# Kernel optimization log

Hardware: AMD Instinct MI355X
Metric: run time of the kernel (lower is better)

The kernel has to match this reference:

```python
import jax, jax.numpy as jnp
import numpy as np

BN_EPS = 1e-5
OUT_H, OUT_W = 32, 32  # crop_size / output_stride = 512/16


def setup_inputs() -> dict:
    key = jax.random.key(0)
    k1, k2, k3, k4 = jax.random.split(key, 4)
    x = jax.random.normal(k1, (16, 2048, 32, 32), dtype=jnp.float32)
    # conv1x1 weight, bias-free: [dim_out, dim_in]
    W = jax.random.normal(k2, (256, 2048), dtype=jnp.float32) * (1.0 / np.sqrt(2048.0))
    gamma = jax.random.normal(k3, (256,), dtype=jnp.float32) * 0.1 + 1.0
    beta = jax.random.normal(k4, (256,), dtype=jnp.float32) * 0.1
    return {"x": x, "W": W, "gamma": gamma, "beta": beta}


def reference(x, W, gamma, beta):
    # 1x1 conv, no bias: channel contraction
    y = jnp.einsum("nchw,oc->nohw", x, W)  # [N, dim_out, H, W]
    # BatchNorm2d in training mode: batch statistics over (N, H, W), biased var
    mean = jnp.mean(y, axis=(0, 2, 3), keepdims=True)
    var = jnp.mean(jnp.square(y - mean), axis=(0, 2, 3), keepdims=True)
    g = gamma.reshape(1, -1, 1, 1)
    b = beta.reshape(1, -1, 1, 1)
    y = g * (y - mean) * jax.lax.rsqrt(var + BN_EPS) + b
    # global average pool to 1x1
    pooled = jnp.mean(y, axis=(2, 3), keepdims=True)  # [N, dim_out, 1, 1]
    # adaptive avg pool from 1x1 to (OUT_H, OUT_W) is a pure broadcast
    out = jnp.broadcast_to(pooled, pooled.shape[:2] + (OUT_H, OUT_W))
    return out
```

## Files before the change

### kernel.cpp

```cpp
#include <hip/hip_runtime.h>
#include <hip/hip_bf16.h>
#include <stdint.h>

#define NB   16
#define CIN  2048
#define OUTC 256
#define HW   1024
#define BJ   64
#define BK   32
#define NJT  (HW / BJ)
#define KSTEPS (CIN / BK)

typedef __attribute__((ext_vector_type(8))) short bf16x8;
typedef __attribute__((ext_vector_type(4))) float f32x4;
typedef __attribute__((ext_vector_type(4))) unsigned int u32x4;

__device__ __forceinline__ unsigned int f2bf(float f) {
    union { float f; unsigned int u; } a; a.f = f;
    return (a.u + 0x7FFFu + ((a.u >> 16) & 1u)) >> 16;
}

__device__ __forceinline__ void block_sync_lds() {
    asm volatile("s_waitcnt lgkmcnt(0)" ::: "memory");
    __builtin_amdgcn_s_barrier();
    asm volatile("" ::: "memory");
}

__global__ void wconv_kernel(const float* __restrict__ W, unsigned short* __restrict__ W16) {
    int i = (blockIdx.x * blockDim.x + threadIdx.x) * 4;
    float4 v = *reinterpret_cast<const float4*>(W + i);
    ushort4 o;
    o.x = (unsigned short)f2bf(v.x);
    o.y = (unsigned short)f2bf(v.y);
    o.z = (unsigned short)f2bf(v.z);
    o.w = (unsigned short)f2bf(v.w);
    *reinterpret_cast<ushort4*>(W16 + i) = o;
}

__global__ __launch_bounds__(512, 2) void gemm_stats_kernel(
    const float* __restrict__ x,
    const unsigned short* __restrict__ W16,
    float* __restrict__ s1_part,
    float* __restrict__ s2_part)
{
    __shared__ __align__(16) unsigned short A0[8192], A1[8192];
    __shared__ __align__(16) unsigned short B0[2048], B1[2048];

    const int tid  = threadIdx.x;
    const int lane = tid & 63;
    const int wave = tid >> 6;
    const int blk  = blockIdx.x;
    const int n    = blk >> 4;
    const int jt   = blk & 15;
    const int j0   = jt * BJ;

    const float* xn = x + (size_t)n * CIN * HW;

    const int arow  = tid >> 1;
    const int ahalf = tid & 1;
    const unsigned short* Agp = W16 + arow * CIN + ahalf * 16;
    const int offA0 = (arow >> 4) * 512 + (arow & 15) * 32 + ((2 * ahalf + 0) ^ (arow & 3)) * 8;
    const int offA1 = (arow >> 4) * 512 + (arow & 15) * 32 + ((2 * ahalf + 1) ^ (arow & 3)) * 8;

    const int bj = tid & 63;
    const int kh = tid >> 6;
    const float* Bgp = xn + (size_t)(kh * 4) * HW + j0 + bj;
    const int offB = (bj >> 4) * 512 + (bj & 15) * 32 + (((kh >> 1)) ^ (bj & 3)) * 8 + (kh & 1) * 4;

    const int rA = lane & 15;
    const int gX = (lane >> 4) ^ (rA & 3);
    const int roffA0 = (2 * wave) * 512 + rA * 32 + gX * 8;
    const int roffA1 = (2 * wave + 1) * 512 + rA * 32 + gX * 8;
    const int roffB  = rA * 32 + gX * 8;

#define LDA(ks, r0, r1) { r0 = *(const u32x4*)(Agp + (ks) * BK); \
                          r1 = *(const u32x4*)(Agp + (ks) * BK + 8); }
#define LDB(ks, f0, f1, f2, f3) { const float* p = Bgp + (size_t)(ks) * BK * HW; \
                                  f0 = p[0]; f1 = p[HW]; f2 = p[2 * HW]; f3 = p[3 * HW]; }
#define WRITE(Ab, Bb, r0, r1, f0, f1, f2, f3) { \
    *(u32x4*)&Ab[offA0] = r0; *(u32x4*)&Ab[offA1] = r1; \
    uint2 pk; pk.x = f2bf(f0) | (f2bf(f1) << 16); pk.y = f2bf(f2) | (f2bf(f3) << 16); \
    *(uint2*)&Bb[offB] = pk; }
#define COMPUTE(Ab, Bb) { \
    bf16x8 af0 = *(const bf16x8*)&Ab[roffA0]; \
    bf16x8 af1 = *(const bf16x8*)&Ab[roffA1]; \
    _Pragma("unroll") \
    for (int ni = 0; ni < 4; ++ni) { \
        bf16x8 bf = *(const bf16x8*)&Bb[ni * 512 + roffB]; \
        acc[0][ni] = __builtin_amdgcn_mfma_f32_16x16x32_bf16(af0, bf, acc[0][ni], 0, 0, 0); \
        acc[1][ni] = __builtin_amdgcn_mfma_f32_16x16x32_bf16(af1, bf, acc[1][ni], 0, 0, 0); \
    } }

    f32x4 acc[2][4] = {};
    u32x4 a00, a01, a10, a11;
    float b00, b01, b02, b03, b10, b11, b12, b13;

    LDA(0, a00, a01); LDB(0, b00, b01, b02, b03);
    LDA(1, a10, a11); LDB(1, b10, b11, b12, b13);
    WRITE(A0, B0, a00, a01, b00, b01, b02, b03);
    LDA(2, a00, a01); LDB(2, b00, b01, b02, b03);
    block_sync_lds();

    #pragma unroll 1
    for (int ks = 0; ks < KSTEPS; ks += 2) {
        COMPUTE(A0, B0);
        {
            WRITE(A1, B1, a10, a11, b10, b11, b12, b13);
            int kp = (ks + 3 < KSTEPS) ? ks + 3 : KSTEPS - 1;
            LDA(kp, a10, a11); LDB(kp, b10, b11, b12, b13);
            block_sync_lds();
        }
        COMPUTE(A1, B1);
        if (ks + 1 < KSTEPS - 1) {
            WRITE(A0, B0, a00, a01, b00, b01, b02, b03);
            int kp = (ks + 4 < KSTEPS) ? ks + 4 : KSTEPS - 1;
            LDA(kp, a00, a01); LDB(kp, b00, b01, b02, b03);
            block_sync_lds();
        }
    }

    float rs[2][4], rq[2][4];
    #pragma unroll
    for (int mi = 0; mi < 2; ++mi) {
        #pragma unroll
        for (int r = 0; r < 4; ++r) {
            float s = 0.f, q = 0.f;
            #pragma unroll
            for (int ni = 0; ni < 4; ++ni) {
                float v = acc[mi][ni][r];
                s += v; q += v * v;
            }
            rs[mi][r] = s; rq[mi][r] = q;
        }
    }
    #pragma unroll
    for (int m = 1; m < 16; m <<= 1) {
        #pragma unroll
        for (int mi = 0; mi < 2; ++mi) {
            #pragma unroll
            for (int r = 0; r < 4; ++r) {
                rs[mi][r] += __shfl_xor(rs[mi][r], m, 64);
                rq[mi][r] += __shfl_xor(rq[mi][r], m, 64);
            }
        }
    }
    if (rA == 0) {
        const int gK = lane >> 4;
        #pragma unroll
        for (int mi = 0; mi < 2; ++mi) {
            #pragma unroll
            for (int r = 0; r < 4; ++r) {
                int o = wave * 32 + mi * 16 + gK * 4 + r;
                s1_part[(jt * NB + n) * OUTC + o] = rs[mi][r];
                s2_part[blk * OUTC + o]           = rq[mi][r];
            }
        }
    }
#undef LDA
#undef LDB
#undef WRITE
#undef COMPUTE
}

__global__ __launch_bounds__(256) void finalize_bcast_kernel(
    const float* __restrict__ s1_part,
    const float* __restrict__ s2_part,
    const float* __restrict__ gamma,
    const float* __restrict__ beta,
    float* __restrict__ out)
{
    const int tid   = threadIdx.x;
    const int slice = tid & 15;
    const int o_l   = tid >> 4;
    const int n0    = blockIdx.x >> 4;
    const int o     = (blockIdx.x & 15) * 16 + o_l;

    float S1 = 0.f, S2 = 0.f;
    #pragma unroll
    for (int q = 0; q < 16; ++q) {
        int p = slice * 16 + q;
        S1 += s1_part[p * OUTC + o];
        S2 += s2_part[p * OUTC + o];
    }
    float s1n = s1_part[(slice * NB + n0) * OUTC + o];
    #pragma unroll
    for (int m = 1; m < 16; m <<= 1) {
        S1  += __shfl_xor(S1, m, 64);
        S2  += __shfl_xor(S2, m, 64);
        s1n += __shfl_xor(s1n, m, 64);
    }
    float mean = S1 * (1.f / 16384.f);
    float var  = S2 * (1.f / 16384.f) - mean * mean;
    float inv  = rsqrtf(var + 1e-5f);
    float v = gamma[o] * (s1n * (1.f / 1024.f) - mean) * inv + beta[o];

    float4 vv = make_float4(v, v, v, v);
    float4* dst = reinterpret_cast<float4*>(out + ((size_t)(n0 * OUTC + o)) * HW);
    #pragma unroll
    for (int it = 0; it < 16; ++it)
        dst[it * 16 + slice] = vv;
}

extern "C" void kernel_launch(void* const* d_in, const int* in_sizes, int n_in,
                              void* d_out, int out_size, void* d_ws, size_t ws_size,
                              hipStream_t stream) {
    const float* x     = (const float*)d_in[0];
    const float* W     = (const float*)d_in[1];
    const float* gamma = (const float*)d_in[2];
    const float* beta  = (const float*)d_in[3];
    float* out = (float*)d_out;

    char* ws = (char*)d_ws;
    unsigned short* W16 = (unsigned short*)ws;
    float* s1_part = (float*)(ws + (1 << 20));
    float* s2_part = (float*)(ws + (1 << 20) + (256 << 10));

    hipLaunchKernelGGL(wconv_kernel, dim3(512), dim3(256), 0, stream, W, W16);
    hipLaunchKernelGGL(gemm_stats_kernel, dim3(256), dim3(512), 0, stream,
                       x, W16, s1_part, s2_part);
    hipLaunchKernelGGL(finalize_bcast_kernel, dim3(NB * (OUTC / 16)), dim3(256), 0, stream,
                       s1_part, s2_part, gamma, beta, out);
}
```

Before: 56.02 us.

## Pre-swizzle weights into MFMA fragment layout and load A directly to registers

The weight prep kernel now writes bf16 weights in MFMA fragment order, so the GEMM kernel loads A operands straight from global/L2 into registers and no longer stages them through LDS. The K step doubles to 64, halving the number of barriers, and only the x tile is staged in LDS. This cuts LDS traffic and sync overhead but raises register use for the A fragments and the prefetched B values, and each block now fetches A directly from L2.

```diff
diff --git a/kernel.cpp b/kernel.cpp
--- a/kernel.cpp
+++ b/kernel.cpp
@@ -7,7 +7,7 @@
 #define OUTC 256
 #define HW   1024
 #define BJ   64
-#define BK   32
+#define BK   64
 #define NJT  (HW / BJ)
 #define KSTEPS (CIN / BK)
 
@@ -26,25 +26,29 @@
     asm volatile("" ::: "memory");
 }
 
-__global__ void wconv_kernel(const float* __restrict__ W, unsigned short* __restrict__ W16) {
-    int i = (blockIdx.x * blockDim.x + threadIdx.x) * 4;
-    float4 v = *reinterpret_cast<const float4*>(W + i);
-    ushort4 o;
-    o.x = (unsigned short)f2bf(v.x);
-    o.y = (unsigned short)f2bf(v.y);
-    o.z = (unsigned short)f2bf(v.z);
-    o.w = (unsigned short)f2bf(v.w);
-    *reinterpret_cast<ushort4*>(W16 + i) = o;
+__global__ void wprep_kernel(const float* __restrict__ W, unsigned short* __restrict__ Afrag) {
+    int g  = blockIdx.x * blockDim.x + threadIdx.x;
+    int o  = g >> 8;
+    int kc = g & 255;
+    const float4* p = reinterpret_cast<const float4*>(W + o * CIN + kc * 8);
+    float4 v0 = p[0], v1 = p[1];
+    u32x4 pk;
+    pk.x = f2bf(v0.x) | (f2bf(v0.y) << 16);
+    pk.y = f2bf(v0.z) | (f2bf(v0.w) << 16);
+    pk.z = f2bf(v1.x) | (f2bf(v1.y) << 16);
+    pk.w = f2bf(v1.z) | (f2bf(v1.w) << 16);
+    int ks32 = kc >> 2, g8 = kc & 3;
+    int lane = g8 * 16 + (o & 15), ot = o >> 4;
+    *reinterpret_cast<u32x4*>(Afrag + (((size_t)ks32 * 16 + ot) * 64 + lane) * 8) = pk;
 }
 
 __global__ __launch_bounds__(512, 2) void gemm_stats_kernel(
     const float* __restrict__ x,
-    const unsigned short* __restrict__ W16,
+    const unsigned short* __restrict__ Afrag,
     float* __restrict__ s1_part,
     float* __restrict__ s2_part)
 {
-    __shared__ __align__(16) unsigned short A0[8192], A1[8192];
-    __shared__ __align__(16) unsigned short B0[2048], B1[2048];
+    __shared__ __align__(16) unsigned short B0[4096], B1[4096];
 
     const int tid  = threadIdx.x;
     const int lane = tid & 63;
@@ -56,65 +60,66 @@
 
     const float* xn = x + (size_t)n * CIN * HW;
 
-    const int arow  = tid >> 1;
-    const int ahalf = tid & 1;
-    const unsigned short* Agp = W16 + arow * CIN + ahalf * 16;
-    const int offA0 = (arow >> 4) * 512 + (arow & 15) * 32 + ((2 * ahalf + 0) ^ (arow & 3)) * 8;
-    const int offA1 = (arow >> 4) * 512 + (arow & 15) * 32 + ((2 * ahalf + 1) ^ (arow & 3)) * 8;
-
     const int bj = tid & 63;
     const int kh = tid >> 6;
-    const float* Bgp = xn + (size_t)(kh * 4) * HW + j0 + bj;
-    const int offB = (bj >> 4) * 512 + (bj & 15) * 32 + (((kh >> 1)) ^ (bj & 3)) * 8 + (kh & 1) * 4;
+    const float* Bgp = xn + (size_t)(kh * 8) * HW + j0 + bj;
+    const int offB = (kh >> 2) * 2048 + (bj >> 4) * 512 + (bj & 15) * 32
+                   + ((kh & 3) ^ (bj & 3)) * 8;
 
     const int rA = lane & 15;
     const int gX = (lane >> 4) ^ (rA & 3);
-    const int roffA0 = (2 * wave) * 512 + rA * 32 + gX * 8;
-    const int roffA1 = (2 * wave + 1) * 512 + rA * 32 + gX * 8;
-    const int roffB  = rA * 32 + gX * 8;
-
-#define LDA(ks, r0, r1) { r0 = *(const u32x4*)(Agp + (ks) * BK); \
-                          r1 = *(const u32x4*)(Agp + (ks) * BK + 8); }
-#define LDB(ks, f0, f1, f2, f3) { const float* p = Bgp + (size_t)(ks) * BK * HW; \
-                                  f0 = p[0]; f1 = p[HW]; f2 = p[2 * HW]; f3 = p[3 * HW]; }
-#define WRITE(Ab, Bb, r0, r1, f0, f1, f2, f3) { \
-    *(u32x4*)&Ab[offA0] = r0; *(u32x4*)&Ab[offA1] = r1; \
-    uint2 pk; pk.x = f2bf(f0) | (f2bf(f1) << 16); pk.y = f2bf(f2) | (f2bf(f3) << 16); \
-    *(uint2*)&Bb[offB] = pk; }
-#define COMPUTE(Ab, Bb) { \
-    bf16x8 af0 = *(const bf16x8*)&Ab[roffA0]; \
-    bf16x8 af1 = *(const bf16x8*)&Ab[roffA1]; \
-    _Pragma("unroll") \
-    for (int ni = 0; ni < 4; ++ni) { \
-        bf16x8 bf = *(const bf16x8*)&Bb[ni * 512 + roffB]; \
-        acc[0][ni] = __builtin_amdgcn_mfma_f32_16x16x32_bf16(af0, bf, acc[0][ni], 0, 0, 0); \
-        acc[1][ni] = __builtin_amdgcn_mfma_f32_16x16x32_bf16(af1, bf, acc[1][ni], 0, 0, 0); \
-    } }
+    const int roffB = rA * 32 + gX * 8;
+
+    const unsigned short* Ab = Afrag + (size_t)lane * 8;
+
+#define LDA(ks, R) { _Pragma("unroll") \
+    for (int h = 0; h < 2; ++h) _Pragma("unroll") for (int t = 0; t < 2; ++t) \
+        R[h * 2 + t] = *(const u32x4*)(Ab + ((((ks) * 2 + h) * 16 + 2 * wave + t) * 64) * 8); }
+#define LDB(ks, F) { const float* p = Bgp + (size_t)(ks) * BK * HW; \
+    _Pragma("unroll") for (int i = 0; i < 8; ++i) F[i] = p[(size_t)i * HW]; }
+#define WRITEB(Bb, F) { u32x4 pk; \
+    pk.x = f2bf(F[0]) | (f2bf(F[1]) << 16); pk.y = f2bf(F[2]) | (f2bf(F[3]) << 16); \
+    pk.z = f2bf(F[4]) | (f2bf(F[5]) << 16); pk.w = f2bf(F[6]) | (f2bf(F[7]) << 16); \
+    *(u32x4*)&Bb[offB] = pk; }
+#define COMPUTE(Bb, R) { _Pragma("unroll") \
+    for (int h = 0; h < 2; ++h) { \
+        bf16x8 af0 = *(const bf16x8*)&R[h * 2 + 0]; \
+        bf16x8 af1 = *(const bf16x8*)&R[h * 2 + 1]; \
+        _Pragma("unroll") \
+        for (int ni = 0; ni < 4; ++ni) { \
+            bf16x8 bf = *(const bf16x8*)&Bb[h * 2048 + ni * 512 + roffB]; \
+            acc[0][ni] = __builtin_amdgcn_mfma_f32_16x16x32_bf16(af0, bf, acc[0][ni], 0, 0, 0); \
+            acc[1][ni] = __builtin_amdgcn_mfma_f32_16x16x32_bf16(af1, bf, acc[1][ni], 0, 0, 0); \
+    } } }
 
     f32x4 acc[2][4] = {};
-    u32x4 a00, a01, a10, a11;
-    float b00, b01, b02, b03, b10, b11, b12, b13;
-
-    LDA(0, a00, a01); LDB(0, b00, b01, b02, b03);
-    LDA(1, a10, a11); LDB(1, b10, b11, b12, b13);
-    WRITE(A0, B0, a00, a01, b00, b01, b02, b03);
-    LDA(2, a00, a01); LDB(2, b00, b01, b02, b03);
+    u32x4 Aa0[4], Aa1[4];
+    float Bs0[8], Bs1[8];
+
+    LDA(0, Aa0); LDB(0, Bs0);
+    LDA(1, Aa1); LDB(1, Bs1);
+    WRITEB(B0, Bs0);
+    LDB(2, Bs0);
     block_sync_lds();
 
     #pragma unroll 1
     for (int ks = 0; ks < KSTEPS; ks += 2) {
-        COMPUTE(A0, B0);
+        COMPUTE(B0, Aa0);
         {
-            WRITE(A1, B1, a10, a11, b10, b11, b12, b13);
-            int kp = (ks + 3 < KSTEPS) ? ks + 3 : KSTEPS - 1;
-            LDA(kp, a10, a11); LDB(kp, b10, b11, b12, b13);
+            int ka = (ks + 2 < KSTEPS) ? ks + 2 : KSTEPS - 1;
+            LDA(ka, Aa0);
+            WRITEB(B1, Bs1);
+            int kb = (ks + 3 < KSTEPS) ? ks + 3 : KSTEPS - 1;
+            LDB(kb, Bs1);
             block_sync_lds();
         }
-        COMPUTE(A1, B1);
-        if (ks + 1 < KSTEPS - 1) {
-            WRITE(A0, B0, a00, a01, b00, b01, b02, b03);
-            int kp = (ks + 4 < KSTEPS) ? ks + 4 : KSTEPS - 1;
-            LDA(kp, a00, a01); LDB(kp, b00, b01, b02, b03);
+        COMPUTE(B1, Aa1);
+        if (ks + 2 < KSTEPS) {
+            int ka = (ks + 3 < KSTEPS) ? ks + 3 : KSTEPS - 1;
+            LDA(ka, Aa1);
+            WRITEB(B0, Bs0);
+            int kb = (ks + 4 < KSTEPS) ? ks + 4 : KSTEPS - 1;
+            LDB(kb, Bs0);
             block_sync_lds();
         }
     }
@@ -158,7 +163,7 @@
     }
 #undef LDA
 #undef LDB
-#undef WRITE
+#undef WRITEB
 #undef COMPUTE
 }
 
@@ -211,13 +216,13 @@
     float* out = (float*)d_out;
 
     char* ws = (char*)d_ws;
-    unsigned short* W16 = (unsigned short*)ws;
+    unsigned short* Afrag = (unsigned short*)ws;
     float* s1_part = (float*)(ws + (1 << 20));
     float* s2_part = (float*)(ws + (1 << 20) + (256 << 10));
 
-    hipLaunchKernelGGL(wconv_kernel, dim3(512), dim3(256), 0, stream, W, W16);
+    hipLaunchKernelGGL(wprep_kernel, dim3(256), dim3(256), 0, stream, W, Afrag);
     hipLaunchKernelGGL(gemm_stats_kernel, dim3(256), dim3(512), 0, stream,
-                       x, W16, s1_part, s2_part);
+                       x, Afrag, s1_part, s2_part);
     hipLaunchKernelGGL(finalize_bcast_kernel, dim3(NB * (OUTC / 16)), dim3(256), 0, stream,
                        s1_part, s2_part, gamma, beta, out);
 }
```

New measurement: 49.15 us. 12.3% less time.
